# Kernel tuning notes

Hardware: AMD Instinct MI355X
Metric: run time of the kernel (lower is better)

The kernel has to match this reference:

```python
import jax, jax.numpy as jnp
import numpy as np

B, P = 512, 256          # batch, n_assets
MAX_W = 0.1              # max_weight from __init__
EPS = 1e-8               # config.EPSILON
N_PGD = 250              # projected-gradient iterations (QP solve)
N_BISECT = 30            # bisection iterations for simplex projection
N_POWER = 20             # power iterations for spectral norm


def setup_inputs() -> dict:
    key = jax.random.key(0)
    k1, k2 = jax.random.split(key, 2)
    A = jax.random.normal(k1, (B, P, P), jnp.float32)
    # PSD covariance, as required by cp.Parameter(PSD=True)
    sigma = jnp.einsum('bij,bkj->bik', A, A) / P + 1e-3 * jnp.eye(P, dtype=jnp.float32)
    beta = jax.random.uniform(k2, (B, P), jnp.float32)  # nonneg risk budgets
    w_prev = jnp.full((B, P), 1.0 / P, jnp.float32)     # default equal weight
    return {
        'sigma': sigma,
        'beta': beta,
        'w_prev': w_prev,
        'log_lambda1': jnp.float32(-3.0),
        'log_lambda2': jnp.float32(-2.0),
    }


def _project_capped_simplex(v, c):
    """Euclidean projection onto {w : sum w = 1, 0 <= w <= c}, batched over leading dims.
    Solves sum(clip(v - tau, 0, c)) = 1 for tau by bisection (monotone decreasing)."""
    lo = v.min(-1, keepdims=True) - c
    hi = v.max(-1, keepdims=True)

    def body(i, carry):
        lo, hi = carry
        tau = 0.5 * (lo + hi)
        s = jnp.clip(v - tau, 0.0, c).sum(-1, keepdims=True)
        too_big = s > 1.0
        return (jnp.where(too_big, tau, lo), jnp.where(too_big, hi, tau))

    lo, hi = jax.lax.fori_loop(0, N_BISECT, body, (lo, hi))
    tau = 0.5 * (lo + hi)
    return jnp.clip(v - tau, 0.0, c)


def _solve_qp(sigma, beta, w_prev, lam1, lam2):
    """min_w  w'Pw - beta'w + lam1*||w||_1 + lam2*||w - w_prev||^2
       s.t.   sum w = 1, 0 <= w <= MAX_W
    via projected gradient descent (on the feasible set w>=0, ||w||_1 = sum w,
    so lam1 contributes a constant lam1 to the gradient)."""
    # step size 1/L with L = 2*lambda_max(P) + 2*lam2, estimated by power iteration
    S = jax.lax.stop_gradient(sigma)
    v = jnp.full((B, P), 1.0 / np.sqrt(P), sigma.dtype)

    def pbody(i, v):
        u = jnp.einsum('bij,bj->bi', S, v)
        return u / (jnp.linalg.norm(u, axis=-1, keepdims=True) + EPS)

    v = jax.lax.fori_loop(0, N_POWER, pbody, v)
    lmax = jnp.einsum('bi,bij,bj->b', v, S, v)                    # [B]
    step = jax.lax.stop_gradient(1.0 / (2.0 * lmax + 2.0 * lam2 + 1e-6))  # [B]

    w0 = jnp.full((B, P), 1.0 / P, sigma.dtype)

    def pgd(w, _):
        g = (2.0 * jnp.einsum('bij,bj->bi', sigma, w)
             - beta + lam1 + 2.0 * lam2 * (w - w_prev))
        w = _project_capped_simplex(w - step[:, None] * g, MAX_W)
        return w, None

    w, _ = jax.lax.scan(pgd, w0, None, length=N_PGD)
    return w


def reference(sigma, beta, w_prev, log_lambda1, log_lambda2):
    lam1 = jnp.exp(log_lambda1)
    lam2 = jnp.exp(log_lambda2)
    w = _solve_qp(sigma, beta, w_prev, lam1, lam2)
    # post-processing from forward(): clamp then renormalize
    w = jnp.clip(w, 0.0, MAX_W)
    return w / (w.sum(-1, keepdims=True) + EPS)
```

## Files before the change

### kernel.cpp

```cpp
#include <hip/hip_runtime.h>
#include <math.h>


#define PP    256
#define MAXW  0.1f
#define EPSF  1e-8f
#define NPGD  250
#define NPOW  10
#define NILLMAX 10
#define FTOL  4e-6f
#define STOPTOL 1e-6f
#define MINIT 20

#define R3S   272
#define TJS   68
#define WRDS  72
#define VCOPY 280

typedef float v2 __attribute__((ext_vector_type(2)));
typedef float v4t __attribute__((ext_vector_type(4)));

template<int CTRL>
__device__ __forceinline__ float dpp_zero(float x) {
    return __int_as_float(__builtin_amdgcn_update_dpp(
        0, __float_as_int(x), CTRL, 0xF, 0xF, true));
}
template<int CTRL>
__device__ __forceinline__ float dpp_keep(float x) {
    int xi = __float_as_int(x);
    return __int_as_float(__builtin_amdgcn_update_dpp(xi, xi, CTRL, 0xF, 0xF, false));
}
__device__ __forceinline__ float rdlane63(float x) {
    return __int_as_float(__builtin_amdgcn_readlane(__float_as_int(x), 63));
}
__device__ __forceinline__ float wave_sum63(float s) {
    s += dpp_zero<0x111>(s);
    s += dpp_zero<0x112>(s);
    s += dpp_zero<0x114>(s);
    s += dpp_zero<0x118>(s);
    s += dpp_zero<0x142>(s);
    s += dpp_zero<0x143>(s);
    return s;
}
__device__ __forceinline__ float wave_min63(float m) {
    m = fminf(m, dpp_keep<0x111>(m));
    m = fminf(m, dpp_keep<0x112>(m));
    m = fminf(m, dpp_keep<0x114>(m));
    m = fminf(m, dpp_keep<0x118>(m));
    m = fminf(m, dpp_keep<0x142>(m));
    m = fminf(m, dpp_keep<0x143>(m));
    return m;
}
__device__ __forceinline__ float wave_max63(float m) {
    m = fmaxf(m, dpp_keep<0x111>(m));
    m = fmaxf(m, dpp_keep<0x112>(m));
    m = fmaxf(m, dpp_keep<0x114>(m));
    m = fmaxf(m, dpp_keep<0x118>(m));
    m = fmaxf(m, dpp_keep<0x142>(m));
    m = fmaxf(m, dpp_keep<0x143>(m));
    return m;
}

__global__ __launch_bounds__(256, 2)
__attribute__((amdgpu_waves_per_eu(2, 2)))
void drb_kernel(const float* __restrict__ sigma,
                const float* __restrict__ beta,
                const float* __restrict__ wprev,
                const float* __restrict__ pl1,
                const float* __restrict__ pl2,
                float* __restrict__ out)
{
    const int b    = blockIdx.x;
    const int tid  = threadIdx.x;
    const int lane = tid & 63;
    const int wv   = tid >> 6;
    const int ti   = tid >> 2;
    const int tj   = tid & 3;

    __shared__ __align__(16) float sigR3[64 * R3S];
    __shared__ __align__(16) float wcop[4 * VCOPY];
    __shared__ __align__(16) float stage[2][256];

    const float* Sb = sigma + (size_t)b * (PP * PP);

    v2 s0[32], s1[32], s2[32];
    {
        const float* r0 = Sb + (4 * ti + 0) * PP + 64 * tj;
#pragma unroll
        for (int k = 0; k < 16; ++k) {
            v4t t = *(const v4t*)(r0 + 4 * k);
            s0[2*k]   = __builtin_shufflevector(t, t, 0, 1);
            s0[2*k+1] = __builtin_shufflevector(t, t, 2, 3);
        }
    }
    {
        const float* r1 = Sb + (4 * ti + 1) * PP + 64 * tj;
#pragma unroll
        for (int k = 0; k < 16; ++k) {
            v4t t = *(const v4t*)(r1 + 4 * k);
            s1[2*k]   = __builtin_shufflevector(t, t, 0, 1);
            s1[2*k+1] = __builtin_shufflevector(t, t, 2, 3);
        }
    }
    {
        const float* r2 = Sb + (4 * ti + 2) * PP + 64 * tj;
#pragma unroll
        for (int k = 0; k < 16; ++k) {
            v4t t = *(const v4t*)(r2 + 4 * k);
            s2[2*k]   = __builtin_shufflevector(t, t, 0, 1);
            s2[2*k+1] = __builtin_shufflevector(t, t, 2, 3);
        }
    }
    {
        const float* r3 = Sb + (4 * ti + 3) * PP + 64 * tj;
        float* d3 = sigR3 + ti * R3S + TJS * tj;
#pragma unroll
        for (int k = 0; k < 16; ++k)
            *(v4t*)(d3 + 4 * k) = *(const v4t*)(r3 + 4 * k);
    }

    const float bt   = beta[b * PP + tid];
    const float wp   = wprev[b * PP + tid];
    const float lam1 = expf(pl1[0]);
    const float lam2 = expf(pl2[0]);

    float* wme = wcop + wv * VCOPY;
    const int wst = 4 * lane + 8 * (lane >> 4);
    const float* wrd = wme + WRDS * tj;

    auto matvec = [&]() -> float {
        v2 y0a = {0.f, 0.f}, y0b = {0.f, 0.f};
        v2 y1a = {0.f, 0.f}, y1b = {0.f, 0.f};
        v2 y2a = {0.f, 0.f}, y2b = {0.f, 0.f};
        v2 y3a = {0.f, 0.f}, y3b = {0.f, 0.f};
        const float* p3 = sigR3 + ti * R3S + TJS * tj;
#pragma unroll
        for (int k = 0; k < 16; ++k) {
            v4t wq = *(const v4t*)(wrd + 4 * k);
            v2 w01 = __builtin_shufflevector(wq, wq, 0, 1);
            v2 w23 = __builtin_shufflevector(wq, wq, 2, 3);
            y0a = __builtin_elementwise_fma(s0[2*k],   w01, y0a);
            y0b = __builtin_elementwise_fma(s0[2*k+1], w23, y0b);
            y1a = __builtin_elementwise_fma(s1[2*k],   w01, y1a);
            y1b = __builtin_elementwise_fma(s1[2*k+1], w23, y1b);
            y2a = __builtin_elementwise_fma(s2[2*k],   w01, y2a);
            y2b = __builtin_elementwise_fma(s2[2*k+1], w23, y2b);
            v4t q = *(const v4t*)(p3 + 4 * k);
            v2 q01 = __builtin_shufflevector(q, q, 0, 1);
            v2 q23 = __builtin_shufflevector(q, q, 2, 3);
            y3a = __builtin_elementwise_fma(q01, w01, y3a);
            y3b = __builtin_elementwise_fma(q23, w23, y3b);
        }
        float r0 = (y0a.x + y0a.y) + (y0b.x + y0b.y);
        float r1 = (y1a.x + y1a.y) + (y1b.x + y1b.y);
        float r2 = (y2a.x + y2a.y) + (y2b.x + y2b.y);
        float r3 = (y3a.x + y3a.y) + (y3b.x + y3b.y);
        r0 += dpp_zero<0x4E>(r0); r1 += dpp_zero<0x4E>(r1);
        r2 += dpp_zero<0x4E>(r2); r3 += dpp_zero<0x4E>(r3);
        r0 += dpp_zero<0xB1>(r0); r1 += dpp_zero<0xB1>(r1);
        r2 += dpp_zero<0xB1>(r2); r3 += dpp_zero<0xB1>(r3);
        float a01 = (tj & 1) ? r1 : r0;
        float a23 = (tj & 1) ? r3 : r2;
        return (tj & 2) ? a23 : a01;
    };

    {
        v4t c = {0.0625f, 0.0625f, 0.0625f, 0.0625f};
        *(v4t*)(wme + wst) = c;
    }

    float y_last = 0.f, a_last = 1.f;
#pragma unroll 1
    for (int pi = 0; pi < NPOW; ++pi) {
        float y = matvec();
        stage[pi & 1][tid] = y;
        __syncthreads();
        v4t u4 = *(const v4t*)(&stage[pi & 1][4 * lane]);
        float ss = fmaf(u4.x, u4.x, fmaf(u4.y, u4.y, fmaf(u4.z, u4.z, u4.w * u4.w)));
        float a  = 1.f / (sqrtf(rdlane63(wave_sum63(ss))) + EPSF);
        v4t n4 = {a * u4.x, a * u4.y, a * u4.z, a * u4.w};
        *(v4t*)(wme + wst) = n4;
        y_last = y; a_last = a;
    }

    float stepf, bmom;
    {
        float ysv = matvec();
        float p   = (a_last * y_last) * ysv;
        stage[0][tid] = p;
        __syncthreads();
        v4t p4 = *(const v4t*)(&stage[0][4 * lane]);
        float lmax = rdlane63(wave_sum63((p4.x + p4.y) + (p4.z + p4.w)));
        float Lsafe = 1.15f * (2.f * lmax + 2.f * lam2) + 1e-6f;
        stepf = 1.f / Lsafe;
        float mu = 2.f * lam2 + 2e-3f;
        float q  = sqrtf(mu / Lsafe);
        bmom = (1.f - q) / (1.f + q);
        __syncthreads();
    }

    float w_own = 1.f / 256.f;
    float z_own = 1.f / 256.f;
    {
        v4t c = {1.f/256.f, 1.f/256.f, 1.f/256.f, 1.f/256.f};
        *(v4t*)(wme + wst) = c;
    }
    const float Ac = 1.f - 2.f * lam2 * stepf;
    const float Bc = -2.f * stepf;
    const float Cc = stepf * (bt - lam1 + 2.f * lam2 * wp);

    float tau_pred = 0.f;
    float tau_last = 0.f;
    float dtau_last = 0.f;

    v4t w4_prev = {1.f/256.f, 1.f/256.f, 1.f/256.f, 1.f/256.f};
    float dm1 = 1.f, dm2 = 1.f;

#pragma unroll 1
    for (int it = 0; it < NPGD; ++it) {
        if (it >= MINIT && dm1 < STOPTOL && dm2 < STOPTOL) break;
        const float bm = (dm1 > 2.0f * dm2) ? 0.f : bmom;

        float y = matvec();
        float v_own = fmaf(z_own, Ac, fmaf(y, Bc, Cc));
        const int sb = it & 1;
        stage[sb][tid] = v_own;
        __syncthreads();

        __builtin_amdgcn_s_setprio(1);
        v4t v4 = *(const v4t*)(&stage[sb][4 * lane]);

        float tau = tau_pred;
        {
            float d0 = v4.x - tau, d1 = v4.y - tau;
            float d2 = v4.z - tau, d3 = v4.w - tau;
            float c0 = __builtin_amdgcn_fmed3f(d0, 0.f, MAXW);
            float c1 = __builtin_amdgcn_fmed3f(d1, 0.f, MAXW);
            float c2 = __builtin_amdgcn_fmed3f(d2, 0.f, MAXW);
            float c3 = __builtin_amdgcn_fmed3f(d3, 0.f, MAXW);
            float Sw = wave_sum63((c0 + c1) + (c2 + c3));
            float f  = rdlane63(Sw) - 1.f;

            if (!(fabsf(f) <= FTOL)) {
                float mnl = fminf(fminf(v4.x, v4.y), fminf(v4.z, v4.w));
                float mxl = fmaxf(fmaxf(v4.x, v4.y), fmaxf(v4.z, v4.w));
                float n0 = ((d0 > 0.f) & (d0 < MAXW)) ? 1.f : 0.f;
                float n1 = ((d1 > 0.f) & (d1 < MAXW)) ? 1.f : 0.f;
                float n2 = ((d2 > 0.f) & (d2 < MAXW)) ? 1.f : 0.f;
                float n3 = ((d3 > 0.f) & (d3 < MAXW)) ? 1.f : 0.f;
                float mnw = wave_min63(mnl);
                float mxw = wave_max63(mxl);
                float Nw  = wave_sum63((n0 + n1) + (n2 + n3));
                float mn  = rdlane63(mnw);
                float mx  = rdlane63(mxw);
                float cnt = rdlane63(Nw);
                bool pos0 = f > 0.f;
                float lo  = pos0 ? tau : mn - MAXW;
                float flo = pos0 ? f   : 256.f * MAXW - 1.f;
                float hi  = pos0 ? mx  : tau;
                float fhi = pos0 ? -1.f : f;
                int side  = pos0 ? 1 : -1;
#pragma unroll 1
                for (int r = 1; r < NILLMAX; ++r) {
                    float tn = fmaf(f, __builtin_amdgcn_rcpf(cnt), tau);
                    float ts = (lo * fhi - hi * flo) *
                               __builtin_amdgcn_rcpf(fhi - flo);
                    bool good = (tn > lo) & (tn < hi);
                    tau = good ? tn : ts;
                    float e0 = v4.x - tau, e1 = v4.y - tau;
                    float e2 = v4.z - tau, e3 = v4.w - tau;
                    float g0 = __builtin_amdgcn_fmed3f(e0, 0.f, MAXW);
                    float g1 = __builtin_amdgcn_fmed3f(e1, 0.f, MAXW);
                    float g2 = __builtin_amdgcn_fmed3f(e2, 0.f, MAXW);
                    float g3 = __builtin_amdgcn_fmed3f(e3, 0.f, MAXW);
                    float m0 = ((e0 > 0.f) & (e0 < MAXW)) ? 1.f : 0.f;
                    float m1 = ((e1 > 0.f) & (e1 < MAXW)) ? 1.f : 0.f;
                    float m2 = ((e2 > 0.f) & (e2 < MAXW)) ? 1.f : 0.f;
                    float m3 = ((e3 > 0.f) & (e3 < MAXW)) ? 1.f : 0.f;
                    float Sr = wave_sum63((g0 + g1) + (g2 + g3));
                    float Nr = wave_sum63((m0 + m1) + (m2 + m3));
                    f   = rdlane63(Sr) - 1.f;
                    cnt = rdlane63(Nr);
                    if (fabsf(f) <= FTOL) break;
                    bool pos = f > 0.f;
                    float nflo = pos ? f   : ((side < 0) ? 0.5f * flo : flo);
                    float nfhi = pos ? ((side > 0) ? 0.5f * fhi : fhi) : f;
                    lo  = pos ? tau : lo;
                    hi  = pos ? hi  : tau;
                    flo = nflo; fhi = nfhi;
                    side = pos ? 1 : -1;
                }
            }
        }

        {
            float dtau = tau - tau_last;
            float rho  = dtau * __builtin_amdgcn_rcpf(dtau_last);
            bool okx = (fabsf(dtau_last) > 1e-20f) & (rho > 0.f) &
                       (rho < 0.9f) & (fabsf(dtau) < 1e-2f);
            float extr = okx ? dtau * rho * __builtin_amdgcn_rcpf(1.f - rho) : 0.f;
            tau_pred = tau + extr;
            tau_last = tau;
            dtau_last = dtau;
        }

        v4t w4n = {__builtin_amdgcn_fmed3f(v4.x - tau, 0.f, MAXW),
                   __builtin_amdgcn_fmed3f(v4.y - tau, 0.f, MAXW),
                   __builtin_amdgcn_fmed3f(v4.z - tau, 0.f, MAXW),
                   __builtin_amdgcn_fmed3f(v4.w - tau, 0.f, MAXW)};
        v4t z4 = {fmaf(bm, w4n.x - w4_prev.x, w4n.x),
                  fmaf(bm, w4n.y - w4_prev.y, w4n.y),
                  fmaf(bm, w4n.z - w4_prev.z, w4n.z),
                  fmaf(bm, w4n.w - w4_prev.w, w4n.w)};
        *(v4t*)(wme + wst) = z4;
        __builtin_amdgcn_s_setprio(0);
        float w_new = __builtin_amdgcn_fmed3f(v_own - tau, 0.f, MAXW);
        z_own = fmaf(bm, w_new - w_own, w_new);
        w_own = w_new;

        {
            float pm = fmaxf(fmaxf(fabsf(w4n.x - w4_prev.x),
                                   fabsf(w4n.y - w4_prev.y)),
                             fmaxf(fabsf(w4n.z - w4_prev.z),
                                   fabsf(w4n.w - w4_prev.w)));
            w4_prev = w4n;
            dm2 = dm1;
            dm1 = rdlane63(wave_max63(pm));
        }
    }

    __syncthreads();
    stage[0][tid] = w_own;
    __syncthreads();
    v4t w4 = *(const v4t*)(&stage[0][4 * lane]);
    float S = rdlane63(wave_sum63((w4.x + w4.y) + (w4.z + w4.w)));
    out[b * PP + tid] = w_own / (S + EPSF);
}

extern "C" void kernel_launch(void* const* d_in, const int* in_sizes, int n_in,
                              void* d_out, int out_size, void* d_ws, size_t ws_size,
                              hipStream_t stream) {
    const float* sigma  = (const float*)d_in[0];
    const float* beta   = (const float*)d_in[1];
    const float* wprevp = (const float*)d_in[2];
    const float* pl1    = (const float*)d_in[3];
    const float* pl2    = (const float*)d_in[4];
    float* outp = (float*)d_out;
    drb_kernel<<<dim3(512), dim3(256), 0, stream>>>(sigma, beta, wprevp, pl1, pl2, outp);
}
```

Before: 272.4 us.

## Warm-start PGD from clipped diagonal solve and drop wave priority hints

The solver no longer starts from equal weights. It uses a diagonal (Jacobi-like) estimate, clipping (beta - lam1 + 2*lam2*w_prev) / (2*sigma_ii + 2*lam2) to [0, MAXW], so the early-exit convergence test is meant to fire after fewer iterations. The minimum iteration count drops from 20 to 16, and the s_setprio raise and lower around the projection section are removed. The start point is not on the simplex, so the first projection may need more bisection steps. Early stopping could also change the result slightly relative to the reference.

```diff
diff --git a/kernel.cpp b/kernel.cpp
--- a/kernel.cpp
+++ b/kernel.cpp
@@ -10,7 +10,7 @@
 #define NILLMAX 10
 #define FTOL  4e-6f
 #define STOPTOL 1e-6f
-#define MINIT 20
+#define MINIT 16
 
 #define R3S   272
 #define TJS   68
@@ -199,11 +199,36 @@
         __syncthreads();
     }
 
-    float w_own = 1.f / 256.f;
-    float z_own = 1.f / 256.f;
-    {
-        v4t c = {1.f/256.f, 1.f/256.f, 1.f/256.f, 1.f/256.f};
-        *(v4t*)(wme + wst) = c;
+    const float den_c = 2.f * lam2;
+    float w_own, z_own;
+    {
+        float sdt = Sb[(size_t)tid * 257];
+        w_own = __builtin_amdgcn_fmed3f(
+            (bt - lam1 + den_c * wp) * __builtin_amdgcn_rcpf(2.f * sdt + den_c),
+            0.f, MAXW);
+        z_own = w_own;
+    }
+    v4t w04;
+    {
+        v4t bt4 = *(const v4t*)(beta  + b * PP + 4 * lane);
+        v4t wp4 = *(const v4t*)(wprev + b * PP + 4 * lane);
+        float sd0 = Sb[(size_t)(4 * lane + 0) * 257];
+        float sd1 = Sb[(size_t)(4 * lane + 1) * 257];
+        float sd2 = Sb[(size_t)(4 * lane + 2) * 257];
+        float sd3 = Sb[(size_t)(4 * lane + 3) * 257];
+        w04.x = __builtin_amdgcn_fmed3f(
+            (bt4.x - lam1 + den_c * wp4.x) * __builtin_amdgcn_rcpf(2.f * sd0 + den_c),
+            0.f, MAXW);
+        w04.y = __builtin_amdgcn_fmed3f(
+            (bt4.y - lam1 + den_c * wp4.y) * __builtin_amdgcn_rcpf(2.f * sd1 + den_c),
+            0.f, MAXW);
+        w04.z = __builtin_amdgcn_fmed3f(
+            (bt4.z - lam1 + den_c * wp4.z) * __builtin_amdgcn_rcpf(2.f * sd2 + den_c),
+            0.f, MAXW);
+        w04.w = __builtin_amdgcn_fmed3f(
+            (bt4.w - lam1 + den_c * wp4.w) * __builtin_amdgcn_rcpf(2.f * sd3 + den_c),
+            0.f, MAXW);
+        *(v4t*)(wme + wst) = w04;
     }
     const float Ac = 1.f - 2.f * lam2 * stepf;
     const float Bc = -2.f * stepf;
@@ -213,7 +238,7 @@
     float tau_last = 0.f;
     float dtau_last = 0.f;
 
-    v4t w4_prev = {1.f/256.f, 1.f/256.f, 1.f/256.f, 1.f/256.f};
+    v4t w4_prev = w04;
     float dm1 = 1.f, dm2 = 1.f;
 
 #pragma unroll 1
@@ -227,7 +252,6 @@
         stage[sb][tid] = v_own;
         __syncthreads();
 
-        __builtin_amdgcn_s_setprio(1);
         v4t v4 = *(const v4t*)(&stage[sb][4 * lane]);
 
         float tau = tau_pred;
@@ -313,7 +337,6 @@
                   fmaf(bm, w4n.z - w4_prev.z, w4n.z),
                   fmaf(bm, w4n.w - w4_prev.w, w4n.w)};
         *(v4t*)(wme + wst) = z4;
-        __builtin_amdgcn_s_setprio(0);
         float w_new = __builtin_amdgcn_fmed3f(v_own - tau, 0.f, MAXW);
         z_own = fmaf(bm, w_new - w_own, w_new);
         w_own = w_new;
```

Result: slower. 278.3 us (+2.2%).
